# Performance work log

Hardware: AMD Instinct MI355X
Metric: run time of the kernel (lower is better)

Reference implementation:

```python
import jax, jax.numpy as jnp
import numpy as np

N_NODES = 200000
D_IN = 256
D_OUT = 256
B = 4096
K1 = 25   # layer-1 fanout
K2 = 10   # layer-2 fanout
M = B * (1 + K2)  # layer-1 node set size: batch centers + their sampled neighbors


def setup_inputs() -> dict:
    key = jax.random.key(0)
    k1, k2, k3, k4, k5, k6 = jax.random.split(key, 6)
    features = jax.random.normal(k1, (N_NODES, D_IN), dtype=jnp.float32)
    # SageLayer weights: [out, 2*in] (concat path, gcn=False); small kaiming-like scale
    W1 = jax.random.normal(k2, (D_OUT, 2 * D_IN), dtype=jnp.float32) * 0.05
    W2 = jax.random.normal(k3, (D_OUT, 2 * D_OUT), dtype=jnp.float32) * 0.05
    nodes_batch = jax.random.randint(k4, (B,), 0, N_NODES, dtype=jnp.int64)
    neigh2 = jax.random.randint(k5, (B, K2), 0, N_NODES, dtype=jnp.int64)
    neigh1 = jax.random.randint(k6, (M, K1), 0, N_NODES, dtype=jnp.int64)
    return {"features": features, "W1": W1, "W2": W2,
            "nodes_batch": nodes_batch, "neigh2": neigh2, "neigh1": neigh1}


def reference(features, W1, W2, nodes_batch, neigh2, neigh1):
    # Layer-1 node set: centers first, then their sampled layer-2 neighbors.
    l1_nodes = jnp.concatenate([nodes_batch, neigh2.reshape(-1)])  # [M]
    # ---- layer 1: MEAN aggregate over K1 sampled neighbors (gather + mean) ----
    agg1 = jnp.mean(features[neigh1], axis=1)          # [M, K1, D_IN] -> [M, D_IN]
    self1 = features[l1_nodes]                         # [M, D_IN]
    # SageLayer: relu(W.mm(cat(self, agg).T)).T == relu(cat @ W.T)
    h1 = jax.nn.relu(jnp.concatenate([self1, agg1], axis=1) @ W1.T)  # [M, D_OUT]
    # ---- layer 2: centers are h1[:B]; neighbor embeddings are h1[B:] in blocks of K2 ----
    nb = nodes_batch.shape[0]
    agg2 = jnp.mean(h1[nb:].reshape(nb, -1, h1.shape[1]), axis=1)    # [B, D_OUT]
    h2 = jax.nn.relu(jnp.concatenate([h1[:nb], agg2], axis=1) @ W2.T)  # [B, D_OUT]
    return h2
```

## Files before the change

### kernel.cpp

```cpp
#include <hip/hip_runtime.h>
#include <hip/hip_bf16.h>

typedef __attribute__((ext_vector_type(8))) short bf16x8;
typedef __attribute__((ext_vector_type(4))) float f32x4;
typedef __attribute__((ext_vector_type(2))) float f32x2;

#define B_SZ   4096
#define K1     25
#define K2     10
#define M_L1   45056
#define D      256
#define K_DIM  512
#define N_NODES 200000

static __device__ __forceinline__ unsigned short f2bf(float f) {
    union { float f; unsigned u; } v; v.f = f;
    return (unsigned short)((v.u + 0x7fffu + ((v.u >> 16) & 1u)) >> 16);
}
static __device__ __forceinline__ float bf2f(unsigned short h) {
    union { unsigned u; float f; } v; v.u = ((unsigned)h) << 16;
    return v.f;
}

__global__ __launch_bounds__(256)
void convert_all(const float* __restrict__ f, unsigned* __restrict__ f8,
                 const float* __restrict__ W1, const float* __restrict__ W2,
                 unsigned short* __restrict__ W1b, unsigned short* __restrict__ W2b) {
    const size_t i = ((size_t)blockIdx.x * 256 + threadIdx.x) * 8;
    const float4 a = *(const float4*)(f + i);
    const float4 b = *(const float4*)(f + i + 4);
    unsigned u0 = 0, u1 = 0;
    u0 = __builtin_amdgcn_cvt_pk_fp8_f32(a.x, a.y, u0, false);
    u0 = __builtin_amdgcn_cvt_pk_fp8_f32(a.z, a.w, u0, true);
    u1 = __builtin_amdgcn_cvt_pk_fp8_f32(b.x, b.y, u1, false);
    u1 = __builtin_amdgcn_cvt_pk_fp8_f32(b.z, b.w, u1, true);
    uint2 r; r.x = u0; r.y = u1;
    *(uint2*)(f8 + (i >> 2)) = r;
    const int j = blockIdx.x * 256 + threadIdx.x;
    if (j < D * K_DIM) {
        W1b[j] = f2bf(W1[j]);
        W2b[j] = f2bf(W2[j]);
    }
}

__global__ __launch_bounds__(512, 4)
void fused_l1(const float* __restrict__ feat,
              const unsigned* __restrict__ f8,
              const int* __restrict__ nodes_batch,
              const int* __restrict__ neigh2,
              const int* __restrict__ neigh1,
              const unsigned short* __restrict__ W,
              unsigned short* __restrict__ h1) {
    __shared__ unsigned short As[32 * 512];
    const int tid  = threadIdx.x;
    const int w    = tid >> 6, lane = tid & 63;
    const int quad = lane >> 4, l16 = lane & 15;
    const int wm   = (w >> 2) << 4;
    const int wn   = (w & 3) << 6;
    const size_t row0 = (size_t)blockIdx.x * 32;

    const unsigned short* bBase = W + (size_t)(wn + l16) * K_DIM + (quad << 3);

    bf16x8 bp[2][8];
    #pragma unroll
    for (int ks = 0; ks < 2; ++ks)
        #pragma unroll
        for (int i = 0; i < 4; ++i)
            bp[0][ks * 4 + i] = *(const bf16x8*)(bBase + (size_t)(i * 16) * K_DIM + ks * 32);

    #pragma unroll 2
    for (int rr = 0; rr < 4; ++rr) {
        const int r = (w << 2) + rr;
        const int m = (int)row0 + r;
        const int self_node = (m < B_SZ) ? nodes_batch[m] : neigh2[m - B_SZ];
        const int* nb = neigh1 + (size_t)m * K1;
        int idxv = (lane < K1) ? nb[lane] : 0;
        const float4 s = *(const float4*)(feat + (size_t)self_node * D + (lane << 2));
        unsigned q[K1];
        #pragma unroll
        for (int j = 0; j < K1; ++j) {
            const int node = __shfl(idxv, j);
            q[j] = f8[(size_t)node * (D / 4) + lane];
        }
        float a0 = 0.f, a1 = 0.f, a2 = 0.f, a3 = 0.f;
        #pragma unroll
        for (int j = 0; j < K1; ++j) {
            const f32x2 lo = __builtin_amdgcn_cvt_pk_f32_fp8(q[j], false);
            const f32x2 hi = __builtin_amdgcn_cvt_pk_f32_fp8(q[j], true);
            a0 += lo.x; a1 += lo.y; a2 += hi.x; a3 += hi.y;
        }
        const float inv = 1.0f / (float)K1;
        const int e0 = lane << 2;
        const int p0 = (e0 >> 3) ^ (r & 7);
        *(ushort4*)&As[r * 512 + (p0 << 3) + (e0 & 7)] =
            make_ushort4(f2bf(s.x), f2bf(s.y), f2bf(s.z), f2bf(s.w));
        const int e1 = D + (lane << 2);
        const int p1 = (e1 >> 3) ^ (r & 7);
        *(ushort4*)&As[r * 512 + (p1 << 3) + (e1 & 7)] =
            make_ushort4(f2bf(a0 * inv), f2bf(a1 * inv), f2bf(a2 * inv), f2bf(a3 * inv));
    }

    __syncthreads();

    f32x4 acc[4];
    #pragma unroll
    for (int j = 0; j < 4; ++j) acc[j] = (f32x4){0.f, 0.f, 0.f, 0.f};

    #pragma unroll
    for (int t = 0; t < 8; ++t) {
        if (t < 7) {
            #pragma unroll
            for (int ks = 0; ks < 2; ++ks)
                #pragma unroll
                for (int i = 0; i < 4; ++i)
                    bp[(t + 1) & 1][ks * 4 + i] =
                        *(const bf16x8*)(bBase + (size_t)(i * 16) * K_DIM + (t + 1) * 64 + ks * 32);
        }
        #pragma unroll
        for (int ks = 0; ks < 2; ++ks) {
            const int row = wm + l16;
            const int ch  = (t << 3) + (ks << 2) + quad;
            const bf16x8 af = *(const bf16x8*)&As[row * 512 + ((ch ^ (row & 7)) << 3)];
            #pragma unroll
            for (int ni = 0; ni < 4; ++ni)
                acc[ni] = __builtin_amdgcn_mfma_f32_16x16x32_bf16(
                    af, bp[t & 1][ks * 4 + ni], acc[ni], 0, 0, 0);
        }
    }

    #pragma unroll
    for (int ni = 0; ni < 4; ++ni)
        #pragma unroll
        for (int rg = 0; rg < 4; ++rg) {
            const size_t gm = row0 + wm + quad * 4 + rg;
            const size_t gn = (size_t)wn + ni * 16 + l16;
            float v = acc[ni][rg];
            v = v > 0.f ? v : 0.f;
            h1[gm * D + gn] = f2bf(v);
        }
}

__global__ __launch_bounds__(256, 4)
void fused_l2(const unsigned short* __restrict__ h1,
              const unsigned short* __restrict__ W,
              float* __restrict__ out) {
    __shared__ unsigned short As[16 * 512];
    const int tid  = threadIdx.x;
    const int w    = tid >> 6, lane = tid & 63;
    const int quad = lane >> 4, l16 = lane & 15;
    const int wn   = w << 6;
    const size_t row0 = (size_t)blockIdx.x * 16;

    const unsigned short* bBase = W + (size_t)(wn + l16) * K_DIM + (quad << 3);

    bf16x8 bp[2][8];
    #pragma unroll
    for (int ks = 0; ks < 2; ++ks)
        #pragma unroll
        for (int i = 0; i < 4; ++i)
            bp[0][ks * 4 + i] = *(const bf16x8*)(bBase + (size_t)(i * 16) * K_DIM + ks * 32);

    #pragma unroll 2
    for (int rr = 0; rr < 4; ++rr) {
        const int r = (w << 2) + rr;
        const size_t b = row0 + r;
        const ushort4 sv = *(const ushort4*)&h1[b * D + (lane << 2)];
        float a0 = 0.f, a1 = 0.f, a2 = 0.f, a3 = 0.f;
        #pragma unroll
        for (int k = 0; k < K2; ++k) {
            const ushort4 v = *(const ushort4*)&h1[(size_t)(B_SZ + b * K2 + k) * D + (lane << 2)];
            a0 += bf2f(v.x); a1 += bf2f(v.y); a2 += bf2f(v.z); a3 += bf2f(v.w);
        }
        const float inv = 1.0f / (float)K2;
        const int e0 = lane << 2;
        const int p0 = (e0 >> 3) ^ (r & 7);
        *(ushort4*)&As[r * 512 + (p0 << 3) + (e0 & 7)] = sv;
        const int e1 = D + (lane << 2);
        const int p1 = (e1 >> 3) ^ (r & 7);
        *(ushort4*)&As[r * 512 + (p1 << 3) + (e1 & 7)] =
            make_ushort4(f2bf(a0 * inv), f2bf(a1 * inv), f2bf(a2 * inv), f2bf(a3 * inv));
    }

    __syncthreads();

    f32x4 acc[4];
    #pragma unroll
    for (int j = 0; j < 4; ++j) acc[j] = (f32x4){0.f, 0.f, 0.f, 0.f};

    #pragma unroll
    for (int t = 0; t < 8; ++t) {
        if (t < 7) {
            #pragma unroll
            for (int ks = 0; ks < 2; ++ks)
                #pragma unroll
                for (int i = 0; i < 4; ++i)
                    bp[(t + 1) & 1][ks * 4 + i] =
                        *(const bf16x8*)(bBase + (size_t)(i * 16) * K_DIM + (t + 1) * 64 + ks * 32);
        }
        #pragma unroll
        for (int ks = 0; ks < 2; ++ks) {
            const int row = l16;
            const int ch  = (t << 3) + (ks << 2) + quad;
            const bf16x8 af = *(const bf16x8*)&As[row * 512 + ((ch ^ (row & 7)) << 3)];
            #pragma unroll
            for (int ni = 0; ni < 4; ++ni)
                acc[ni] = __builtin_amdgcn_mfma_f32_16x16x32_bf16(
                    af, bp[t & 1][ks * 4 + ni], acc[ni], 0, 0, 0);
        }
    }

    #pragma unroll
    for (int ni = 0; ni < 4; ++ni)
        #pragma unroll
        for (int rg = 0; rg < 4; ++rg) {
            const size_t gm = row0 + quad * 4 + rg;
            const size_t gn = (size_t)wn + ni * 16 + l16;
            float v = acc[ni][rg];
            out[gm * D + gn] = v > 0.f ? v : 0.f;
        }
}

extern "C" void kernel_launch(void* const* d_in, const int* in_sizes, int n_in,
                              void* d_out, int out_size, void* d_ws, size_t ws_size,
                              hipStream_t stream) {
    const float* feat        = (const float*)d_in[0];
    const float* W1          = (const float*)d_in[1];
    const float* W2          = (const float*)d_in[2];
    const int*   nodes_batch = (const int*)d_in[3];
    const int*   neigh2      = (const int*)d_in[4];
    const int*   neigh1      = (const int*)d_in[5];
    float* out = (float*)d_out;

    char* ws = (char*)d_ws;
    unsigned*       f8  = (unsigned*)(ws);
    unsigned short* h1  = (unsigned short*)(ws + 51200000);
    unsigned short* W1b = (unsigned short*)(ws + 51200000 + 23068672);
    unsigned short* W2b = (unsigned short*)(ws + 51200000 + 23068672 + 262144);

    convert_all<<<25000, 256, 0, stream>>>(feat, f8, W1, W2, W1b, W2b);
    fused_l1<<<M_L1 / 32, 512, 0, stream>>>(feat, f8, nodes_batch, neigh2, neigh1, W1b, h1);
    fused_l2<<<B_SZ / 16, 256, 0, stream>>>(h1, W2b, out);
}
```

Before: 441.5 us.

## Gather fp8 neighbor rows directly into LDS and shrink layer-1 tiles

Layer-1 neighbor gathers now use global_load_lds to write each fp8 neighbor row straight into a per-wave LDS staging buffer, with neighbor indices read via readlane, instead of holding 25 register loads per lane. The layer-1 block shrinks from 32 rows and 512 threads to 16 rows and 256 threads. The weight double-buffer prefetch is dropped in both layers, and weights are now loaded just in time inside each k-step. The goal is to cut register pressure and raise occupancy so more gathers are in flight, at the cost of more weight reloads per output row and exposed weight-load latency.

```diff
diff --git a/kernel.cpp b/kernel.cpp
--- a/kernel.cpp
+++ b/kernel.cpp
@@ -12,6 +12,9 @@
 #define D      256
 #define K_DIM  512
 #define N_NODES 200000
+
+#define AS1 __attribute__((address_space(1)))
+#define AS3 __attribute__((address_space(3)))
 
 static __device__ __forceinline__ unsigned short f2bf(float f) {
     union { float f; unsigned u; } v; v.f = f;
@@ -43,7 +46,7 @@
     }
 }
 
-__global__ __launch_bounds__(512, 4)
+__global__ __launch_bounds__(256, 4)
 void fused_l1(const float* __restrict__ feat,
               const unsigned* __restrict__ f8,
               const int* __restrict__ nodes_batch,
@@ -51,42 +54,39 @@
               const int* __restrict__ neigh1,
               const unsigned short* __restrict__ W,
               unsigned short* __restrict__ h1) {
-    __shared__ unsigned short As[32 * 512];
+    __shared__ unsigned short As[16 * 512];
+    __shared__ unsigned stage[4][K1 * 64];
     const int tid  = threadIdx.x;
     const int w    = tid >> 6, lane = tid & 63;
     const int quad = lane >> 4, l16 = lane & 15;
-    const int wm   = (w >> 2) << 4;
-    const int wn   = (w & 3) << 6;
-    const size_t row0 = (size_t)blockIdx.x * 32;
-
-    const unsigned short* bBase = W + (size_t)(wn + l16) * K_DIM + (quad << 3);
-
-    bf16x8 bp[2][8];
-    #pragma unroll
-    for (int ks = 0; ks < 2; ++ks)
-        #pragma unroll
-        for (int i = 0; i < 4; ++i)
-            bp[0][ks * 4 + i] = *(const bf16x8*)(bBase + (size_t)(i * 16) * K_DIM + ks * 32);
-
-    #pragma unroll 2
+    const int wn   = w << 6;
+    const size_t row0 = (size_t)blockIdx.x * 16;
+
     for (int rr = 0; rr < 4; ++rr) {
         const int r = (w << 2) + rr;
         const int m = (int)row0 + r;
-        const int self_node = (m < B_SZ) ? nodes_batch[m] : neigh2[m - B_SZ];
-        const int* nb = neigh1 + (size_t)m * K1;
-        int idxv = (lane < K1) ? nb[lane] : 0;
+        int self_node = (m < B_SZ) ? nodes_batch[m] : neigh2[m - B_SZ];
+        self_node = __builtin_amdgcn_readfirstlane(self_node);
         const float4 s = *(const float4*)(feat + (size_t)self_node * D + (lane << 2));
-        unsigned q[K1];
+        const int iv = (lane < K1) ? neigh1[(size_t)m * K1 + lane] : 0;
+
+        asm volatile("s_waitcnt lgkmcnt(0)" ::: "memory");
         #pragma unroll
         for (int j = 0; j < K1; ++j) {
-            const int node = __shfl(idxv, j);
-            q[j] = f8[(size_t)node * (D / 4) + lane];
-        }
+            const int n = __builtin_amdgcn_readlane(iv, j);
+            __builtin_amdgcn_global_load_lds(
+                (const AS1 void*)(f8 + (size_t)n * (D / 4) + lane),
+                (AS3 void*)(&stage[w][j * 64]), 4, 0, 0);
+        }
+        asm volatile("s_waitcnt vmcnt(0)" ::: "memory");
+        __builtin_amdgcn_sched_barrier(0);
+
         float a0 = 0.f, a1 = 0.f, a2 = 0.f, a3 = 0.f;
         #pragma unroll
         for (int j = 0; j < K1; ++j) {
-            const f32x2 lo = __builtin_amdgcn_cvt_pk_f32_fp8(q[j], false);
-            const f32x2 hi = __builtin_amdgcn_cvt_pk_f32_fp8(q[j], true);
+            const unsigned qj = stage[w][j * 64 + lane];
+            const f32x2 lo = __builtin_amdgcn_cvt_pk_f32_fp8(qj, false);
+            const f32x2 hi = __builtin_amdgcn_cvt_pk_f32_fp8(qj, true);
             a0 += lo.x; a1 += lo.y; a2 += hi.x; a3 += hi.y;
         }
         const float inv = 1.0f / (float)K1;
@@ -102,29 +102,27 @@
 
     __syncthreads();
 
+    const unsigned short* bBase = W + (size_t)(wn + l16) * K_DIM + (quad << 3);
     f32x4 acc[4];
     #pragma unroll
     for (int j = 0; j < 4; ++j) acc[j] = (f32x4){0.f, 0.f, 0.f, 0.f};
 
     #pragma unroll
     for (int t = 0; t < 8; ++t) {
-        if (t < 7) {
-            #pragma unroll
-            for (int ks = 0; ks < 2; ++ks)
-                #pragma unroll
-                for (int i = 0; i < 4; ++i)
-                    bp[(t + 1) & 1][ks * 4 + i] =
-                        *(const bf16x8*)(bBase + (size_t)(i * 16) * K_DIM + (t + 1) * 64 + ks * 32);
-        }
+        bf16x8 bp[8];
+        #pragma unroll
+        for (int ks = 0; ks < 2; ++ks)
+            #pragma unroll
+            for (int i = 0; i < 4; ++i)
+                bp[ks * 4 + i] = *(const bf16x8*)(bBase + (size_t)(i * 16) * K_DIM + t * 64 + ks * 32);
         #pragma unroll
         for (int ks = 0; ks < 2; ++ks) {
-            const int row = wm + l16;
-            const int ch  = (t << 3) + (ks << 2) + quad;
-            const bf16x8 af = *(const bf16x8*)&As[row * 512 + ((ch ^ (row & 7)) << 3)];
+            const int ch = (t << 3) + (ks << 2) + quad;
+            const bf16x8 af = *(const bf16x8*)&As[l16 * 512 + ((ch ^ (l16 & 7)) << 3)];
             #pragma unroll
             for (int ni = 0; ni < 4; ++ni)
                 acc[ni] = __builtin_amdgcn_mfma_f32_16x16x32_bf16(
-                    af, bp[t & 1][ks * 4 + ni], acc[ni], 0, 0, 0);
+                    af, bp[ks * 4 + ni], acc[ni], 0, 0, 0);
         }
     }
 
@@ -132,7 +130,7 @@
     for (int ni = 0; ni < 4; ++ni)
         #pragma unroll
         for (int rg = 0; rg < 4; ++rg) {
-            const size_t gm = row0 + wm + quad * 4 + rg;
+            const size_t gm = row0 + quad * 4 + rg;
             const size_t gn = (size_t)wn + ni * 16 + l16;
             float v = acc[ni][rg];
             v = v > 0.f ? v : 0.f;
@@ -151,15 +149,6 @@
     const int wn   = w << 6;
     const size_t row0 = (size_t)blockIdx.x * 16;
 
-    const unsigned short* bBase = W + (size_t)(wn + l16) * K_DIM + (quad << 3);
-
-    bf16x8 bp[2][8];
-    #pragma unroll
-    for (int ks = 0; ks < 2; ++ks)
-        #pragma unroll
-        for (int i = 0; i < 4; ++i)
-            bp[0][ks * 4 + i] = *(const bf16x8*)(bBase + (size_t)(i * 16) * K_DIM + ks * 32);
-
     #pragma unroll 2
     for (int rr = 0; rr < 4; ++rr) {
         const int r = (w << 2) + rr;
@@ -183,29 +172,27 @@
 
     __syncthreads();
 
+    const unsigned short* bBase = W + (size_t)(wn + l16) * K_DIM + (quad << 3);
     f32x4 acc[4];
     #pragma unroll
     for (int j = 0; j < 4; ++j) acc[j] = (f32x4){0.f, 0.f, 0.f, 0.f};
 
     #pragma unroll
     for (int t = 0; t < 8; ++t) {
-        if (t < 7) {
-            #pragma unroll
-            for (int ks = 0; ks < 2; ++ks)
-                #pragma unroll
-                for (int i = 0; i < 4; ++i)
-                    bp[(t + 1) & 1][ks * 4 + i] =
-                        *(const bf16x8*)(bBase + (size_t)(i * 16) * K_DIM + (t + 1) * 64 + ks * 32);
-        }
+        bf16x8 bp[8];
+        #pragma unroll
+        for (int ks = 0; ks < 2; ++ks)
+            #pragma unroll
+            for (int i = 0; i < 4; ++i)
+                bp[ks * 4 + i] = *(const bf16x8*)(bBase + (size_t)(i * 16) * K_DIM + t * 64 + ks * 32);
         #pragma unroll
         for (int ks = 0; ks < 2; ++ks) {
-            const int row = l16;
-            const int ch  = (t << 3) + (ks << 2) + quad;
-            const bf16x8 af = *(const bf16x8*)&As[row * 512 + ((ch ^ (row & 7)) << 3)];
+            const int ch = (t << 3) + (ks << 2) + quad;
+            const bf16x8 af = *(const bf16x8*)&As[l16 * 512 + ((ch ^ (l16 & 7)) << 3)];
             #pragma unroll
             for (int ni = 0; ni < 4; ++ni)
                 acc[ni] = __builtin_amdgcn_mfma_f32_16x16x32_bf16(
-                    af, bp[t & 1][ks * 4 + ni], acc[ni], 0, 0, 0);
+                    af, bp[ks * 4 + ni], acc[ni], 0, 0, 0);
         }
     }
 
@@ -238,6 +225,6 @@
     unsigned short* W2b = (unsigned short*)(ws + 51200000 + 23068672 + 262144);
 
     convert_all<<<25000, 256, 0, stream>>>(feat, f8, W1, W2, W1b, W2b);
-    fused_l1<<<M_L1 / 32, 512, 0, stream>>>(feat, f8, nodes_batch, neigh2, neigh1, W1b, h1);
+    fused_l1<<<M_L1 / 16, 256, 0, stream>>>(feat, f8, nodes_batch, neigh2, neigh1, W1b, h1);
     fused_l2<<<B_SZ / 16, 256, 0, stream>>>(h1, W2b, out);
 }
```

Result: faster. 421.2 us (-4.6%).
